# Kernel tuning notes

Measured on AMD Instinct MI355X. Metric: run time of the kernel, lower is better.

## Reference

```python
import jax, jax.numpy as jnp
import numpy as np

N, E, G = 50000, 800000, 512
F, DE, DG = 64, 16, 32
H, HEADS, C, L, NC = 128, 4, 32, 3, 1
EPS = 1e-5


def _bn(x, g, b, m, v):
    # eval-mode BatchNorm1d with running stats
    return (x - m) / jnp.sqrt(v + EPS) * g + b


def setup_inputs():
    key = jax.random.key(0)
    ks = jax.random.split(key, 24)

    def bn_params(k, d):
        k1, k2, k3, k4 = jax.random.split(k, 4)
        return (1.0 + 0.1 * jax.random.normal(k1, (d,), jnp.float32),
                0.1 * jax.random.normal(k2, (d,), jnp.float32),
                0.1 * jax.random.normal(k3, (d,), jnp.float32),
                jax.random.uniform(k4, (d,), jnp.float32, 0.5, 1.5))

    sc = lambda k, sh, fan: jax.random.normal(k, sh, jnp.float32) / np.float32(np.sqrt(fan))
    inp = {}
    inp['x'] = jax.random.normal(ks[0], (N, F), jnp.float32)
    inp['edge_attr'] = jax.random.normal(ks[1], (E, DE), jnp.float32)
    inp['global_features'] = jax.random.normal(ks[2], (G, DG), jnp.float32)
    inp['edge_index'] = jax.random.randint(ks[3], (2, E), 0, N)
    inp['batch'] = jnp.sort(jax.random.randint(ks[4], (N,), 0, G))
    inp['node_w'] = sc(ks[5], (F, H), F); inp['node_b'] = jnp.zeros((H,), jnp.float32)
    inp['node_bn_g'], inp['node_bn_b'], inp['node_bn_m'], inp['node_bn_v'] = bn_params(ks[6], H)
    inp['edge_w'] = sc(ks[7], (DE, H), DE); inp['edge_b'] = jnp.zeros((H,), jnp.float32)
    inp['glob_w'] = sc(ks[8], (DG, H), DG); inp['glob_b'] = jnp.zeros((H,), jnp.float32)
    inp['glob_bn_g'], inp['glob_bn_b'], inp['glob_bn_m'], inp['glob_bn_v'] = bn_params(ks[9], H)
    inp['gat_lin'] = sc(ks[10], (L, H, HEADS * C), H)
    inp['gat_asrc'] = sc(ks[11], (L, HEADS, C), C)
    inp['gat_adst'] = sc(ks[12], (L, HEADS, C), C)
    inp['gat_bias'] = jnp.zeros((L, H), jnp.float32)
    bg, bb, bm, bv = zip(*[bn_params(jax.random.fold_in(ks[13], i), H) for i in range(L)])
    inp['bn_g'] = jnp.stack(bg); inp['bn_b'] = jnp.stack(bb)
    inp['bn_m'] = jnp.stack(bm); inp['bn_v'] = jnp.stack(bv)
    inp['lin1_w'] = sc(ks[14], (3 * H, H), 3 * H); inp['lin1_b'] = jnp.zeros((H,), jnp.float32)
    inp['lin2_w'] = sc(ks[15], (H, NC), H); inp['lin2_b'] = jnp.zeros((NC,), jnp.float32)
    return inp


def reference(x, edge_attr, global_features, edge_index, batch, node_w, node_b, node_bn_g, node_bn_b, node_bn_m, node_bn_v, edge_w, edge_b, glob_w, glob_b, glob_bn_g, glob_bn_b, glob_bn_m, glob_bn_v, gat_lin, gat_asrc, gat_adst, gat_bias, bn_g, bn_b, bn_m, bn_v, lin1_w, lin1_b, lin2_w, lin2_b):
    n = x.shape[0]
    h = jax.nn.relu(_bn(x @ node_w + node_b, node_bn_g, node_bn_b, node_bn_m, node_bn_v))
    _ = jax.nn.relu(edge_attr @ edge_w + edge_b)  # edge encoder: computed but unused by GATConv, as in source
    # add self loops (PyG GATConv default)
    loops = jnp.arange(n)
    src = jnp.concatenate([edge_index[0], loops])
    dst = jnp.concatenate([edge_index[1], loops])
    for i in range(L):
        identity = h
        hh = (h @ gat_lin[i]).reshape(n, HEADS, C)
        a_src = jnp.einsum('nhc,hc->nh', hh, gat_asrc[i])
        a_dst = jnp.einsum('nhc,hc->nh', hh, gat_adst[i])
        e = jax.nn.leaky_relu(a_src[src] + a_dst[dst], 0.2)  # [E+n, HEADS]
        e_max = jax.ops.segment_max(e, dst, num_segments=n)
        ee = jnp.exp(e - e_max[dst])
        den = jax.ops.segment_sum(ee, dst, num_segments=n)
        alpha = ee / (den[dst] + 1e-16)
        out = jax.ops.segment_sum(hh[src] * alpha[..., None], dst, num_segments=n)
        out = out.reshape(n, HEADS * C) + gat_bias[i]
        out = jax.nn.relu(_bn(out, bn_g[i], bn_b[i], bn_m[i], bn_v[i]))
        h = out + identity  # residual: dims always match (HEADS*C == H)
    g = global_features.shape[0]
    cnt = jax.ops.segment_sum(jnp.ones((n,), h.dtype), batch, num_segments=g)
    x_mean = jax.ops.segment_sum(h, batch, num_segments=g) / jnp.maximum(cnt, 1.0)[:, None]
    x_max = jax.ops.segment_max(h, batch, num_segments=g)
    x_max = jnp.where(jnp.isfinite(x_max), x_max, 0.0)  # guard rare empty graphs
    gfeat = jax.nn.relu(_bn(global_features @ glob_w + glob_b, glob_bn_g, glob_bn_b, glob_bn_m, glob_bn_v))
    z = jnp.concatenate([x_mean, x_max, gfeat], axis=1)
    z = jax.nn.relu(z @ lin1_w + lin1_b)
    return z @ lin2_w + lin2_b
```

## Files before the change

### kernel.cpp

```cpp
#include <hip/hip_runtime.h>
#include <hip/hip_bf16.h>

typedef unsigned short u16;
typedef unsigned int   u32;

#define HD 128
#define FD 64
#define EPS 1e-5f

using bf16x8 = __attribute__((ext_vector_type(8))) short;
using f32x4  = __attribute__((ext_vector_type(4))) float;

__device__ __forceinline__ float b2f(u16 v) { return __uint_as_float(((u32)v) << 16); }
__device__ __forceinline__ u16 f2b(float f) {
    u32 u = __float_as_uint(f);
    return (u16)((u + 0x7FFF + ((u >> 16) & 1)) >> 16);
}
__device__ __forceinline__ float lo16(u32 u) { return __uint_as_float(u << 16); }
__device__ __forceinline__ float hi16(u32 u) { return __uint_as_float(u & 0xFFFF0000u); }

__device__ __forceinline__ bf16x8 pack8(const float* p) {
    bf16x8 r;
    #pragma unroll
    for (int j = 0; j < 8; j++) r[j] = (short)f2b(p[j]);
    return r;
}

__global__ __launch_bounds__(256) void k_hist(const int* __restrict__ dst, int* __restrict__ cnt, int E) {
    int e = blockIdx.x * 256 + threadIdx.x;
    if (e < E) atomicAdd(&cnt[dst[e]], 1);
}

__global__ __launch_bounds__(256) void k_scanA(const int* __restrict__ cnt, int* __restrict__ rowptr,
                                               int* __restrict__ bsum, int N) {
    __shared__ int s[256];
    int tid = threadIdx.x;
    int i = blockIdx.x * 256 + tid;
    s[tid] = (i < N) ? cnt[i] : 0;
    __syncthreads();
    for (int off = 1; off < 256; off <<= 1) {
        int t = (tid >= off) ? s[tid - off] : 0;
        __syncthreads();
        s[tid] += t;
        __syncthreads();
    }
    if (i < N) rowptr[i + 1] = s[tid];
    if (tid == 255) bsum[blockIdx.x] = s[255];
}

__global__ __launch_bounds__(256) void k_scanB(int* __restrict__ bsum, int SB) {
    __shared__ int s[256];
    int tid = threadIdx.x;
    s[tid] = (tid < SB) ? bsum[tid] : 0;
    __syncthreads();
    for (int off = 1; off < 256; off <<= 1) {
        int t = (tid >= off) ? s[tid - off] : 0;
        __syncthreads();
        s[tid] += t;
        __syncthreads();
    }
    if (tid < SB) bsum[tid] = s[tid];
}

__global__ __launch_bounds__(256) void k_scanC(int* __restrict__ rowptr, const int* __restrict__ bsum, int N) {
    int i = blockIdx.x * 256 + threadIdx.x;
    if (i == 0) rowptr[0] = 0;
    if (i < N) {
        int b = i >> 8;
        if (b > 0) rowptr[i + 1] += bsum[b - 1];
    }
}

__global__ __launch_bounds__(256) void k_scatter(const int* __restrict__ src, const int* __restrict__ dst,
                                                 const int* __restrict__ rowptr, int* __restrict__ fill,
                                                 int* __restrict__ colidx, int E) {
    int e = blockIdx.x * 256 + threadIdx.x;
    if (e < E) {
        int d = dst[e];
        int slot = atomicAdd(&fill[d], 1);
        colidx[rowptr[d] + slot] = src[e];
    }
}

__global__ __launch_bounds__(256) void k_wprep(const float* __restrict__ node_w, const float* __restrict__ gat_lin,
                                               u16* __restrict__ wf_node, u16* __restrict__ wf_gat) {
    int y = blockIdx.y;
    const float* src; u16* dst; int K;
    if (y == 0) { src = node_w; dst = wf_node; K = FD; }
    else { src = gat_lin + (size_t)(y - 1) * HD * HD; dst = wf_gat + (size_t)(y - 1) * HD * HD; K = HD; }
    int KT = K >> 5;
    int total = K * HD;
    for (int f = blockIdx.x * 256 + threadIdx.x; f < total; f += gridDim.x * 256) {
        int j = f & 7;
        int lane = (f >> 3) & 63;
        int t = f >> 9;
        int kt = t % KT;
        int ct = t / KT;
        int k = kt * 32 + (lane >> 4) * 8 + j;
        int col = ct * 16 + (lane & 15);
        dst[f] = f2b(src[k * HD + col]);
    }
}

__global__ __launch_bounds__(256) void k_node_mfma(
    const float* __restrict__ x, const u16* __restrict__ wf, const float* __restrict__ bias,
    const float* __restrict__ g, const float* __restrict__ bb, const float* __restrict__ m,
    const float* __restrict__ v, u16* __restrict__ h, int N) {
    int wv = threadIdx.x >> 6, lane = threadIdx.x & 63;
    int rowbase = blockIdx.x * 64 + wv * 16;
    if (rowbase >= N) return;
    int n16 = lane & 15, quad = lane >> 4;
    int arow = min(rowbase + n16, N - 1);
    f32x4 acc[8] = {};
    #pragma unroll
    for (int kt = 0; kt < 2; kt++) {
        bf16x8 a = pack8(x + (size_t)arow * FD + kt * 32 + quad * 8);
        #pragma unroll
        for (int ct = 0; ct < 8; ct++) {
            bf16x8 b = *(const bf16x8*)(wf + ((size_t)(ct * 2 + kt) * 64 + lane) * 8);
            acc[ct] = __builtin_amdgcn_mfma_f32_16x16x32_bf16(a, b, acc[ct], 0, 0, 0);
        }
    }
    #pragma unroll
    for (int ct = 0; ct < 8; ct++) {
        int col = ct * 16 + n16;
        float sc = g[col] * rsqrtf(v[col] + EPS);
        float bi = (bias[col] - m[col]) * sc + bb[col];
        #pragma unroll
        for (int reg = 0; reg < 4; reg++) {
            int row = rowbase + quad * 4 + reg;
            if (row < N) h[(size_t)row * HD + col] = f2b(fmaxf(acc[ct][reg] * sc + bi, 0.f));
        }
    }
}

__global__ __launch_bounds__(256) void k_gat_mfma(
    const u16* __restrict__ h, const u16* __restrict__ wf,
    const float* __restrict__ asrcw, const float* __restrict__ adstw,
    u16* __restrict__ hh, float* __restrict__ a_src, float* __restrict__ a_dst, int N) {
    int wv = threadIdx.x >> 6, lane = threadIdx.x & 63;
    int rowbase = blockIdx.x * 64 + wv * 16;
    if (rowbase >= N) return;
    int n16 = lane & 15, quad = lane >> 4;
    int arow = min(rowbase + n16, N - 1);
    f32x4 acc[8] = {};
    #pragma unroll
    for (int kt = 0; kt < 4; kt++) {
        bf16x8 a = *(const bf16x8*)(h + (size_t)arow * HD + kt * 32 + quad * 8);
        #pragma unroll
        for (int ct = 0; ct < 8; ct++) {
            bf16x8 b = *(const bf16x8*)(wf + ((size_t)(ct * 4 + kt) * 64 + lane) * 8);
            acc[ct] = __builtin_amdgcn_mfma_f32_16x16x32_bf16(a, b, acc[ct], 0, 0, 0);
        }
    }
    float asw[8], adw[8];
    #pragma unroll
    for (int ct = 0; ct < 8; ct++) {
        asw[ct] = asrcw[ct * 16 + n16];
        adw[ct] = adstw[ct * 16 + n16];
    }
    float ps[4][4], pd[4][4];
    #pragma unroll
    for (int hd = 0; hd < 4; hd++)
        #pragma unroll
        for (int reg = 0; reg < 4; reg++) {
            ps[hd][reg] = acc[2 * hd][reg] * asw[2 * hd] + acc[2 * hd + 1][reg] * asw[2 * hd + 1];
            pd[hd][reg] = acc[2 * hd][reg] * adw[2 * hd] + acc[2 * hd + 1][reg] * adw[2 * hd + 1];
        }
    #pragma unroll
    for (int msk = 1; msk < 16; msk <<= 1) {
        #pragma unroll
        for (int hd = 0; hd < 4; hd++)
            #pragma unroll
            for (int reg = 0; reg < 4; reg++) {
                ps[hd][reg] += __shfl_xor(ps[hd][reg], msk);
                pd[hd][reg] += __shfl_xor(pd[hd][reg], msk);
            }
    }
    #pragma unroll
    for (int reg = 0; reg < 4; reg++) {
        int row = rowbase + quad * 4 + reg;
        if (row < N) {
            #pragma unroll
            for (int ct = 0; ct < 8; ct++)
                hh[(size_t)row * HD + ct * 16 + n16] = f2b(acc[ct][reg]);
            if (n16 < 4) {
                float ws = 0.f, wd = 0.f;
                #pragma unroll
                for (int hd = 0; hd < 4; hd++)
                    if (n16 == hd) { ws = ps[hd][reg]; wd = pd[hd][reg]; }
                a_src[row * 4 + n16] = ws;
                a_dst[row * 4 + n16] = wd;
            }
        }
    }
}

__global__ __launch_bounds__(256) void k_agg(
    u16* __restrict__ h, const u32* __restrict__ hh32,
    const float* __restrict__ a_src, const float* __restrict__ a_dst,
    const int* __restrict__ rowptr, const int* __restrict__ colidx,
    const float* __restrict__ bias, const float* __restrict__ bng, const float* __restrict__ bnb,
    const float* __restrict__ bnm, const float* __restrict__ bnv, int N) {
    __shared__ int   sL[4][64];
    __shared__ __align__(16) float eeL[4][64][4];
    int wv = threadIdx.x >> 6, lane = threadIdx.x & 63;
    int node = blockIdx.x * 4 + wv;
    if (node >= N) return;
    int head = lane >> 4;
    const float4* as4p = (const float4*)a_src;
    float4 ad4 = ((const float4*)a_dst)[node];
    float adh = (head == 0) ? ad4.x : (head == 1) ? ad4.y : (head == 2) ? ad4.z : ad4.w;
    float ash = a_src[node * 4 + head];
    float e = ash + adh;
    e = (e > 0.f) ? e : 0.2f * e;
    float ee = __expf(e);
    float den = ee;
    u32 hv = hh32[(size_t)node * 64 + lane];
    float acc0 = ee * lo16(hv), acc1 = ee * hi16(hv);
    int beg = rowptr[node], end = rowptr[node + 1];
    for (int base = beg; base < end; base += 64) {
        int cnt = end - base; if (cnt > 64) cnt = 64;
        int s = 0;
        float4 e4 = {0.f, 0.f, 0.f, 0.f};
        if (lane < cnt) {
            s = colidx[base + lane];
            float4 as4 = as4p[s];
            float t0 = as4.x + ad4.x, t1 = as4.y + ad4.y, t2 = as4.z + ad4.z, t3 = as4.w + ad4.w;
            t0 = (t0 > 0.f) ? t0 : 0.2f * t0; t1 = (t1 > 0.f) ? t1 : 0.2f * t1;
            t2 = (t2 > 0.f) ? t2 : 0.2f * t2; t3 = (t3 > 0.f) ? t3 : 0.2f * t3;
            e4.x = __expf(t0); e4.y = __expf(t1); e4.z = __expf(t2); e4.w = __expf(t3);
        }
        sL[wv][lane] = s;
        ((float4*)eeL[wv][lane])[0] = e4;
        #pragma unroll 4
        for (int j = 0; j < cnt; j++) {
            int sj = sL[wv][j];
            float w = eeL[wv][j][head];
            u32 hv2 = hh32[(size_t)sj * 64 + lane];
            den += w;
            acc0 += w * lo16(hv2);
            acc1 += w * hi16(hv2);
        }
    }
    float inv = 1.0f / (den + 1e-16f);
    int c0 = lane * 2, c1 = c0 + 1;
    float o0 = acc0 * inv, o1 = acc1 * inv;
    float sc0 = bng[c0] * rsqrtf(bnv[c0] + EPS);
    float sc1 = bng[c1] * rsqrtf(bnv[c1] + EPS);
    o0 = (o0 + bias[c0] - bnm[c0]) * sc0 + bnb[c0];
    o1 = (o1 + bias[c1] - bnm[c1]) * sc1 + bnb[c1];
    o0 = fmaxf(o0, 0.f); o1 = fmaxf(o1, 0.f);
    u32 idv = ((const u32*)h)[(size_t)node * 64 + lane];
    o0 += lo16(idv); o1 += hi16(idv);
    ((u32*)h)[(size_t)node * 64 + lane] = ((u32)f2b(o1) << 16) | f2b(o0);
}

__global__ __launch_bounds__(256) void k_pool(
    const u16* __restrict__ h, const int* __restrict__ batch,
    float* __restrict__ z, int N, int G) {
    __shared__ float ssum[128], smax[128];
    int g = blockIdx.x;
    int c = threadIdx.x & 127, half = threadIdx.x >> 7;
    int lo = 0, hi = N;
    while (lo < hi) { int mid = (lo + hi) >> 1; if (batch[mid] < g) lo = mid + 1; else hi = mid; }
    int beg = lo;
    hi = N;
    while (lo < hi) { int mid = (lo + hi) >> 1; if (batch[mid] <= g) lo = mid + 1; else hi = mid; }
    int end = lo;
    float s = 0.f, mx = -3.4e38f;
    for (int r = beg + half; r < end; r += 2) {
        float v = b2f(h[(size_t)r * HD + c]);
        s += v; mx = fmaxf(mx, v);
    }
    if (half == 1) { ssum[c] = s; smax[c] = mx; }
    __syncthreads();
    if (half == 0) {
        s += ssum[c]; mx = fmaxf(mx, smax[c]);
        int cnt = end - beg;
        float mean = s / (float)(cnt > 0 ? cnt : 1);
        if (cnt == 0) mx = 0.f;
        z[(size_t)g * 384 + c] = mean;
        z[(size_t)g * 384 + 128 + c] = mx;
    }
}

__global__ __launch_bounds__(128) void k_glob(
    const float* __restrict__ gf, const float* __restrict__ W, const float* __restrict__ b,
    const float* __restrict__ g_, const float* __restrict__ bb, const float* __restrict__ m_,
    const float* __restrict__ v_, float* __restrict__ z, int G) {
    int g = blockIdx.x, j = threadIdx.x;
    float acc = b[j];
    #pragma unroll 8
    for (int k = 0; k < 32; k++) acc += gf[g * 32 + k] * W[k * HD + j];
    float sc = g_[j] * rsqrtf(v_[j] + EPS);
    acc = (acc - m_[j]) * sc + bb[j];
    z[(size_t)g * 384 + 256 + j] = fmaxf(acc, 0.f);
}

__global__ __launch_bounds__(128) void k_final(
    const float* __restrict__ z, const float* __restrict__ W1, const float* __restrict__ b1,
    const float* __restrict__ W2, const float* __restrict__ b2, float* __restrict__ out, int G) {
    __shared__ float zs[384];
    __shared__ float red[128];
    int g = blockIdx.x, tid = threadIdx.x;
    for (int i = tid; i < 384; i += 128) zs[i] = z[(size_t)g * 384 + i];
    __syncthreads();
    float acc = b1[tid];
    #pragma unroll 4
    for (int k = 0; k < 384; k++) acc += zs[k] * W1[k * HD + tid];
    acc = fmaxf(acc, 0.f);
    red[tid] = acc * W2[tid];
    __syncthreads();
    for (int sft = 64; sft > 0; sft >>= 1) {
        if (tid < sft) red[tid] += red[tid + sft];
        __syncthreads();
    }
    if (tid == 0) out[g] = red[0] + b2[0];
}

extern "C" void kernel_launch(void* const* d_in, const int* in_sizes, int n_in,
                              void* d_out, int out_size, void* d_ws, size_t ws_size,
                              hipStream_t stream) {
    (void)n_in; (void)out_size; (void)ws_size;
    const float* x        = (const float*)d_in[0];
    const float* gfeat    = (const float*)d_in[2];
    const int*   ei       = (const int*)d_in[3];
    const int*   batch    = (const int*)d_in[4];
    const float* node_w   = (const float*)d_in[5];
    const float* node_b   = (const float*)d_in[6];
    const float* nbg      = (const float*)d_in[7];
    const float* nbb      = (const float*)d_in[8];
    const float* nbm      = (const float*)d_in[9];
    const float* nbv      = (const float*)d_in[10];
    const float* glob_w   = (const float*)d_in[13];
    const float* glob_b   = (const float*)d_in[14];
    const float* gbg      = (const float*)d_in[15];
    const float* gbb      = (const float*)d_in[16];
    const float* gbm      = (const float*)d_in[17];
    const float* gbv      = (const float*)d_in[18];
    const float* gat_lin  = (const float*)d_in[19];
    const float* gat_asrc = (const float*)d_in[20];
    const float* gat_adst = (const float*)d_in[21];
    const float* gat_bias = (const float*)d_in[22];
    const float* bn_g     = (const float*)d_in[23];
    const float* bn_b     = (const float*)d_in[24];
    const float* bn_m     = (const float*)d_in[25];
    const float* bn_v     = (const float*)d_in[26];
    const float* lin1_w   = (const float*)d_in[27];
    const float* lin1_b   = (const float*)d_in[28];
    const float* lin2_w   = (const float*)d_in[29];
    const float* lin2_b   = (const float*)d_in[30];

    const int N = in_sizes[0] / FD;
    const int E = in_sizes[3] / 2;
    const int G = in_sizes[2] / 32;
    const int* srcp = ei;
    const int* dstp = ei + E;

    char* p = (char*)d_ws;
    auto alloc = [&](size_t bytes) -> char* {
        char* r = p;
        p += (bytes + 255) & ~(size_t)255;
        return r;
    };
    u16*   h       = (u16*)alloc((size_t)N * HD * 2);
    u16*   hh      = (u16*)alloc((size_t)N * HD * 2);
    float* a_src   = (float*)alloc((size_t)N * 4 * 4);
    float* a_dst   = (float*)alloc((size_t)N * 4 * 4);
    int*   rowptr  = (int*)alloc((size_t)(N + 1) * 4);
    int*   cnt     = (int*)alloc((size_t)N * 4);
    int*   fill    = (int*)alloc((size_t)N * 4);
    int*   bsum    = (int*)alloc(256 * 4);
    int*   colidx  = (int*)alloc((size_t)E * 4);
    float* z       = (float*)alloc((size_t)G * 384 * 4);
    u16*   wf_node = (u16*)alloc((size_t)FD * HD * 2);
    u16*   wf_gat  = (u16*)alloc((size_t)3 * HD * HD * 2);

    hipMemsetAsync(cnt, 0, (size_t)N * 4, stream);
    hipMemsetAsync(fill, 0, (size_t)N * 4, stream);

    k_wprep<<<dim3(32, 4), 256, 0, stream>>>(node_w, gat_lin, wf_node, wf_gat);

    int eb = (E + 255) / 256;
    int SB = (N + 255) / 256;
    k_hist<<<eb, 256, 0, stream>>>(dstp, cnt, E);
    k_scanA<<<SB, 256, 0, stream>>>(cnt, rowptr, bsum, N);
    k_scanB<<<1, 256, 0, stream>>>(bsum, SB);
    k_scanC<<<SB, 256, 0, stream>>>(rowptr, bsum, N);
    k_scatter<<<eb, 256, 0, stream>>>(srcp, dstp, rowptr, fill, colidx, E);

    k_node_mfma<<<(N + 63) / 64, 256, 0, stream>>>(x, wf_node, node_b, nbg, nbb, nbm, nbv, h, N);

    for (int i = 0; i < 3; i++) {
        k_gat_mfma<<<(N + 63) / 64, 256, 0, stream>>>(
            h, wf_gat + (size_t)i * HD * HD,
            gat_asrc + i * HD, gat_adst + i * HD,
            hh, a_src, a_dst, N);
        k_agg<<<(N + 3) / 4, 256, 0, stream>>>(
            h, (const u32*)hh, a_src, a_dst, rowptr, colidx,
            gat_bias + i * HD, bn_g + i * HD, bn_b + i * HD, bn_m + i * HD, bn_v + i * HD, N);
    }

    k_pool<<<G, 256, 0, stream>>>(h, batch, z, N, G);
    k_glob<<<G, 128, 0, stream>>>(gfeat, glob_w, glob_b, gbg, gbb, gbm, gbv, z, G);
    k_final<<<G, 128, 0, stream>>>(z, lin1_w, lin1_b, lin2_w, lin2_b, (float*)d_out, G);
}
```

Baseline: 464.9 us.

## Bin edges by destination range before CSR scatter and fuse readout kernels

Replaces the direct random-scatter CSR build with a two-pass approach: edges are first bucketed by coarse destination bins in shared memory and written contiguously, then each bin block scatters into colidx over a small, cache-local destination range. It also fuses the pool, global-feature MLP and final linear kernels into one readout kernel, and merges the two memsets into one. The aim is to cut scattered global atomics and writes, plus launch count, at the cost of an extra 8-byte-per-edge buffer pass.

New measurement: 436.8 us. -6.0%, faster.

```diff
diff --git a/kernel.cpp b/kernel.cpp
--- a/kernel.cpp
+++ b/kernel.cpp
@@ -3,6 +3,7 @@
 
 typedef unsigned short u16;
 typedef unsigned int   u32;
+typedef unsigned long long u64;
 
 #define HD 128
 #define FD 64
@@ -71,14 +72,77 @@
     }
 }
 
-__global__ __launch_bounds__(256) void k_scatter(const int* __restrict__ src, const int* __restrict__ dst,
-                                                 const int* __restrict__ rowptr, int* __restrict__ fill,
-                                                 int* __restrict__ colidx, int E) {
-    int e = blockIdx.x * 256 + threadIdx.x;
-    if (e < E) {
-        int d = dst[e];
+__global__ __launch_bounds__(256) void k_binA(
+    const int* __restrict__ src, const int* __restrict__ dst, const int* __restrict__ rowptr,
+    int* __restrict__ bcur, u64* __restrict__ binned, int E, int bsh, int NB, int numTiles) {
+    __shared__ u32 os[4096], od[4096];
+    __shared__ int hist[256], obase[256], ofs[256], gpos[256];
+    int tid = threadIdx.x;
+    for (int t = blockIdx.x; t < numTiles; t += gridDim.x) {
+        int base = t * 4096;
+        int cnt = E - base; if (cnt > 4096) cnt = 4096;
+        hist[tid] = 0;
+        __syncthreads();
+        u32 rs[16], rd[16];
+        #pragma unroll
+        for (int r = 0; r < 16; r++) {
+            int li = r * 256 + tid;
+            if (li < cnt) {
+                rs[r] = src[base + li];
+                rd[r] = dst[base + li];
+                atomicAdd(&hist[rd[r] >> bsh], 1);
+            }
+        }
+        __syncthreads();
+        int val = hist[tid];
+        obase[tid] = val;
+        __syncthreads();
+        for (int off = 1; off < 256; off <<= 1) {
+            int t2 = (tid >= off) ? obase[tid - off] : 0;
+            __syncthreads();
+            obase[tid] += t2;
+            __syncthreads();
+        }
+        int excl = obase[tid] - val;
+        __syncthreads();
+        obase[tid] = excl;
+        ofs[tid] = excl;
+        __syncthreads();
+        #pragma unroll
+        for (int r = 0; r < 16; r++) {
+            int li = r * 256 + tid;
+            if (li < cnt) {
+                int b = rd[r] >> bsh;
+                int posn = atomicAdd(&ofs[b], 1);
+                os[posn] = rs[r];
+                od[posn] = rd[r];
+            }
+        }
+        __syncthreads();
+        if (tid < NB && hist[tid] > 0)
+            gpos[tid] = rowptr[tid << bsh] + atomicAdd(&bcur[tid], hist[tid]);
+        __syncthreads();
+        for (int li = tid; li < cnt; li += 256) {
+            u32 d = od[li];
+            int b = d >> bsh;
+            binned[(size_t)gpos[b] + (li - obase[b])] = ((u64)d << 32) | os[li];
+        }
+        __syncthreads();
+    }
+}
+
+__global__ __launch_bounds__(256) void k_binB(
+    const u64* __restrict__ binned, const int* __restrict__ rowptr,
+    int* __restrict__ fill, int* __restrict__ colidx, int N, int bsh) {
+    int b = blockIdx.x;
+    int n0 = b << bsh;
+    int n1 = (b + 1) << bsh; if (n1 > N) n1 = N;
+    int r0 = rowptr[n0], r1 = rowptr[n1];
+    for (int i = r0 + threadIdx.x; i < r1; i += 256) {
+        u64 pk = binned[i];
+        u32 d = (u32)(pk >> 32), s = (u32)pk;
         int slot = atomicAdd(&fill[d], 1);
-        colidx[rowptr[d] + slot] = src[e];
+        colidx[rowptr[d] + slot] = (int)s;
     }
 }
 
@@ -256,12 +320,19 @@
     ((u32*)h)[(size_t)node * 64 + lane] = ((u32)f2b(o1) << 16) | f2b(o0);
 }
 
-__global__ __launch_bounds__(256) void k_pool(
+__global__ __launch_bounds__(256) void k_readout(
     const u16* __restrict__ h, const int* __restrict__ batch,
-    float* __restrict__ z, int N, int G) {
-    __shared__ float ssum[128], smax[128];
-    int g = blockIdx.x;
-    int c = threadIdx.x & 127, half = threadIdx.x >> 7;
+    const float* __restrict__ gf, const float* __restrict__ glob_w, const float* __restrict__ glob_b,
+    const float* __restrict__ gbg, const float* __restrict__ gbb,
+    const float* __restrict__ gbm, const float* __restrict__ gbv,
+    const float* __restrict__ W1, const float* __restrict__ b1,
+    const float* __restrict__ W2, const float* __restrict__ b2,
+    float* __restrict__ out, int N, int G) {
+    __shared__ float zs[384];
+    __shared__ float sA[128], sB[128];
+    __shared__ float pr[256];
+    int g = blockIdx.x, tid = threadIdx.x;
+    int c = tid & 127, half = tid >> 7;
     int lo = 0, hi = N;
     while (lo < hi) { int mid = (lo + hi) >> 1; if (batch[mid] < g) lo = mid + 1; else hi = mid; }
     int beg = lo;
@@ -273,50 +344,38 @@
         float v = b2f(h[(size_t)r * HD + c]);
         s += v; mx = fmaxf(mx, v);
     }
-    if (half == 1) { ssum[c] = s; smax[c] = mx; }
+    if (half == 1) { sA[c] = s; sB[c] = mx; }
     __syncthreads();
     if (half == 0) {
-        s += ssum[c]; mx = fmaxf(mx, smax[c]);
-        int cnt = end - beg;
-        float mean = s / (float)(cnt > 0 ? cnt : 1);
-        if (cnt == 0) mx = 0.f;
-        z[(size_t)g * 384 + c] = mean;
-        z[(size_t)g * 384 + 128 + c] = mx;
-    }
-}
-
-__global__ __launch_bounds__(128) void k_glob(
-    const float* __restrict__ gf, const float* __restrict__ W, const float* __restrict__ b,
-    const float* __restrict__ g_, const float* __restrict__ bb, const float* __restrict__ m_,
-    const float* __restrict__ v_, float* __restrict__ z, int G) {
-    int g = blockIdx.x, j = threadIdx.x;
-    float acc = b[j];
-    #pragma unroll 8
-    for (int k = 0; k < 32; k++) acc += gf[g * 32 + k] * W[k * HD + j];
-    float sc = g_[j] * rsqrtf(v_[j] + EPS);
-    acc = (acc - m_[j]) * sc + bb[j];
-    z[(size_t)g * 384 + 256 + j] = fmaxf(acc, 0.f);
-}
-
-__global__ __launch_bounds__(128) void k_final(
-    const float* __restrict__ z, const float* __restrict__ W1, const float* __restrict__ b1,
-    const float* __restrict__ W2, const float* __restrict__ b2, float* __restrict__ out, int G) {
-    __shared__ float zs[384];
-    __shared__ float red[128];
-    int g = blockIdx.x, tid = threadIdx.x;
-    for (int i = tid; i < 384; i += 128) zs[i] = z[(size_t)g * 384 + i];
-    __syncthreads();
-    float acc = b1[tid];
+        s += sA[c]; mx = fmaxf(mx, sB[c]);
+        int cntn = end - beg;
+        zs[c] = s / (float)(cntn > 0 ? cntn : 1);
+        zs[128 + c] = (cntn == 0) ? 0.f : mx;
+    } else {
+        float acc = glob_b[c];
+        #pragma unroll 8
+        for (int k = 0; k < 32; k++) acc += gf[g * 32 + k] * glob_w[k * HD + c];
+        float sc = gbg[c] * rsqrtf(gbv[c] + EPS);
+        acc = (acc - gbm[c]) * sc + gbb[c];
+        zs[256 + c] = fmaxf(acc, 0.f);
+    }
+    __syncthreads();
+    float acc = (half == 0) ? b1[c] : 0.f;
+    int k0 = half * 192;
     #pragma unroll 4
-    for (int k = 0; k < 384; k++) acc += zs[k] * W1[k * HD + tid];
-    acc = fmaxf(acc, 0.f);
-    red[tid] = acc * W2[tid];
+    for (int k = k0; k < k0 + 192; k++) acc += zs[k] * W1[k * HD + c];
+    pr[tid] = acc;
+    __syncthreads();
+    if (half == 0) {
+        float a = fmaxf(pr[c] + pr[c + 128], 0.f);
+        pr[c] = a * W2[c];
+    }
     __syncthreads();
     for (int sft = 64; sft > 0; sft >>= 1) {
-        if (tid < sft) red[tid] += red[tid + sft];
-        __syncthreads();
-    }
-    if (tid == 0) out[g] = red[0] + b2[0];
+        if (tid < sft) pr[tid] += pr[tid + sft];
+        __syncthreads();
+    }
+    if (tid == 0) out[g] = pr[0] + b2[0];
 }
 
 extern "C" void kernel_launch(void* const* d_in, const int* in_sizes, int n_in,
@@ -358,6 +417,10 @@
     const int* srcp = ei;
     const int* dstp = ei + E;
 
+    int bsh = 8;
+    while (((N + (1 << bsh) - 1) >> bsh) > 256) bsh++;
+    const int NB = (N + (1 << bsh) - 1) >> bsh;
+
     char* p = (char*)d_ws;
     auto alloc = [&](size_t bytes) -> char* {
         char* r = p;
@@ -369,16 +432,18 @@
     float* a_src   = (float*)alloc((size_t)N * 4 * 4);
     float* a_dst   = (float*)alloc((size_t)N * 4 * 4);
     int*   rowptr  = (int*)alloc((size_t)(N + 1) * 4);
+    char*  zbase   = p;
     int*   cnt     = (int*)alloc((size_t)N * 4);
     int*   fill    = (int*)alloc((size_t)N * 4);
+    int*   bcur    = (int*)alloc(256 * 4);
+    size_t zbytes  = (size_t)(p - zbase);
     int*   bsum    = (int*)alloc(256 * 4);
     int*   colidx  = (int*)alloc((size_t)E * 4);
-    float* z       = (float*)alloc((size_t)G * 384 * 4);
+    u64*   binned  = (u64*)alloc((size_t)E * 8);
     u16*   wf_node = (u16*)alloc((size_t)FD * HD * 2);
     u16*   wf_gat  = (u16*)alloc((size_t)3 * HD * HD * 2);
 
-    hipMemsetAsync(cnt, 0, (size_t)N * 4, stream);
-    hipMemsetAsync(fill, 0, (size_t)N * 4, stream);
+    hipMemsetAsync(zbase, 0, zbytes, stream);
 
     k_wprep<<<dim3(32, 4), 256, 0, stream>>>(node_w, gat_lin, wf_node, wf_gat);
 
@@ -388,7 +453,11 @@
     k_scanA<<<SB, 256, 0, stream>>>(cnt, rowptr, bsum, N);
     k_scanB<<<1, 256, 0, stream>>>(bsum, SB);
     k_scanC<<<SB, 256, 0, stream>>>(rowptr, bsum, N);
-    k_scatter<<<eb, 256, 0, stream>>>(srcp, dstp, rowptr, fill, colidx, E);
+
+    int numTiles = (E + 4095) / 4096;
+    int binAGrid = numTiles < 512 ? numTiles : 512;
+    k_binA<<<binAGrid, 256, 0, stream>>>(srcp, dstp, rowptr, bcur, binned, E, bsh, NB, numTiles);
+    k_binB<<<NB, 256, 0, stream>>>(binned, rowptr, fill, colidx, N, bsh);
 
     k_node_mfma<<<(N + 63) / 64, 256, 0, stream>>>(x, wf_node, node_b, nbg, nbb, nbm, nbv, h, N);
 
@@ -402,7 +471,6 @@
             gat_bias + i * HD, bn_g + i * HD, bn_b + i * HD, bn_m + i * HD, bn_v + i * HD, N);
     }
 
-    k_pool<<<G, 256, 0, stream>>>(h, batch, z, N, G);
-    k_glob<<<G, 128, 0, stream>>>(gfeat, glob_w, glob_b, gbg, gbb, gbm, gbv, z, G);
-    k_final<<<G, 128, 0, stream>>>(z, lin1_w, lin1_b, lin2_w, lin2_b, (float*)d_out, G);
-}
+    k_readout<<<G, 256, 0, stream>>>(h, batch, gfeat, glob_w, glob_b, gbg, gbb, gbm, gbv,
+                                     lin1_w, lin1_b, lin2_w, lin2_b, (float*)d_out, N, G);
+}
```
